# Optimization experiments

Hardware: AMD Instinct MI355X
Metric: run time of the kernel (lower is better)

Reference implementation:

```python
import jax, jax.numpy as jnp
import numpy as np

N = 100000
E = 1600000
D_IN = 128
HID = 128
N_CLASSES = 40
NEG_SLOPE = 0.2  # PyG GATConv default
BN_EPS = 1e-5


def setup_inputs() -> dict:
    key = jax.random.key(0)
    ks = jax.random.split(key, 16)
    s = 0.1
    return {
        "x": jax.random.normal(ks[0], (N, D_IN), dtype=jnp.float32),
        "edge_index": jax.random.randint(ks[1], (2, E), 0, N, dtype=jnp.int64),
        # GAT layer 1 (in=D_IN, out=HID, heads=1)
        "W1": jax.random.normal(ks[2], (D_IN, HID), dtype=jnp.float32) * s,
        "a_src1": jax.random.normal(ks[3], (HID,), dtype=jnp.float32) * s,
        "a_dst1": jax.random.normal(ks[4], (HID,), dtype=jnp.float32) * s,
        "b1": jnp.zeros((HID,), dtype=jnp.float32),
        # GAT layer 2 (in=HID, out=HID, heads=1)
        "W2": jax.random.normal(ks[5], (HID, HID), dtype=jnp.float32) * s,
        "a_src2": jax.random.normal(ks[6], (HID,), dtype=jnp.float32) * s,
        "a_dst2": jax.random.normal(ks[7], (HID,), dtype=jnp.float32) * s,
        "b2": jnp.zeros((HID,), dtype=jnp.float32),
        # shared BatchNorm1d(HID) applied after every conv
        "gamma": jnp.ones((HID,), dtype=jnp.float32),
        "beta": jnp.zeros((HID,), dtype=jnp.float32),
        # output Linear(HID, N_CLASSES)
        "Wout": jax.random.normal(ks[8], (HID, N_CLASSES), dtype=jnp.float32) * s,
        "bout": jnp.zeros((N_CLASSES,), dtype=jnp.float32),
    }


def reference(x, edge_index, W1, a_src1, a_dst1, b1, W2, a_src2, a_dst2, b2,
              gamma, beta, Wout, bout):
    n = x.shape[0]
    loops = jnp.arange(n, dtype=edge_index.dtype)  # add_self_loops (GATConv default)
    src = jnp.concatenate([edge_index[0], loops])
    dst = jnp.concatenate([edge_index[1], loops])

    def gat_layer(h_in, W, a_s, a_d, b):
        h = h_in @ W                                   # [N, HID]
        e_src = h @ a_s                                # [N] per-node src score
        e_dst = h @ a_d                                # [N] per-node dst score
        e = jax.nn.leaky_relu(e_src[src] + e_dst[dst], NEG_SLOPE)  # [E+N]
        # segment softmax over incoming edges of each dst node
        m = jax.ops.segment_max(e, dst, num_segments=n)
        p = jnp.exp(e - m[dst])
        denom = jax.ops.segment_sum(p, dst, num_segments=n)
        alpha = p / denom[dst]
        out = jax.ops.segment_sum(alpha[:, None] * h[src], dst, num_segments=n)
        return out + b

    def bn_elu(z):
        mu = z.mean(axis=0)
        var = ((z - mu) ** 2).mean(axis=0)  # biased var (BN training mode)
        zh = (z - mu) / jnp.sqrt(var + BN_EPS) * gamma + beta
        return jax.nn.elu(zh)

    h = bn_elu(gat_layer(x, W1, a_src1, a_dst1, b1))
    h = bn_elu(gat_layer(h, W2, a_src2, a_dst2, b2))
    return h @ Wout + bout
```

## Files before the change

kernel.cpp:

```cpp
#include <hip/hip_runtime.h>

#define NNODES 100000
#define NEDGES 1600000
#define ET (NEDGES + NNODES)
#define NBUCK 196
#define NEG 0.2f
#define BNEPS 1e-5f
#define EPB 16384
#define NBLK_E ((ET + EPB - 1) / EPB)

typedef __attribute__((ext_vector_type(8))) short short8;
typedef __attribute__((ext_vector_type(4))) float floatx4;
typedef __attribute__((ext_vector_type(2))) float floatx2;

__device__ __forceinline__ unsigned short f2b(float x) {
    unsigned int u = __float_as_uint(x);
    u += 0x7fff + ((u >> 16) & 1);
    return (unsigned short)(u >> 16);
}
__device__ __forceinline__ float b2f(unsigned short u) {
    return __uint_as_float(((unsigned int)u) << 16);
}
__device__ __forceinline__ float blo2f(unsigned int v) {
    return __uint_as_float(v << 16);
}
__device__ __forceinline__ float bhi2f(unsigned int v) {
    return __uint_as_float(v & 0xffff0000u);
}
__device__ __forceinline__ floatx2 u2f2(unsigned int v) {
    floatx2 r;
    r.x = __uint_as_float(v << 16);
    r.y = __uint_as_float(v & 0xffff0000u);
    return r;
}

__device__ __forceinline__ int edge_src(const int* ei, int e, int w64) {
    if (e >= NEDGES) return e - NEDGES;
    return w64 ? ei[2 * e] : ei[e];
}
__device__ __forceinline__ int edge_dst(const int* ei, int e, int w64) {
    if (e >= NEDGES) return e - NEDGES;
    return w64 ? ei[2 * (NEDGES + e)] : ei[NEDGES + e];
}

__global__ void k_prep(const float* __restrict__ W1, const float* __restrict__ W2,
                       unsigned short* __restrict__ WT1, unsigned short* __restrict__ WT2,
                       const int* ei, int* flag) {
    int t = blockIdx.x * 256 + threadIdx.x;
    if (t == 0) {
        int is64 = 1;
        for (int j = 1; j < 16; j += 2)
            if (ei[j] != 0) is64 = 0;
        *flag = is64;
    }
    int k = t >> 7, n = t & 127;
    WT1[n * 128 + k] = f2b(W1[t]);
    WT2[n * 128 + k] = f2b(W2[t]);
}

__global__ __launch_bounds__(256) void k_bhist(const int* __restrict__ ei,
                                               const int* flag, int* bcnt) {
    __shared__ int lc[256];
    int t = threadIdx.x;
    lc[t] = 0;
    __syncthreads();
    int w64 = *flag;
    int base = blockIdx.x * EPB;
    for (int j = 0; j < EPB / 256; j++) {
        int e = base + j * 256 + t;
        if (e < ET) atomicAdd(&lc[edge_dst(ei, e, w64) >> 9], 1);
    }
    __syncthreads();
    if (t < NBUCK && lc[t]) atomicAdd(&bcnt[t], lc[t]);
}

__global__ void k_bscan(const int* __restrict__ bcnt, int* bbase, int* bcur) {
    __shared__ int sh[256];
    int t = threadIdx.x;
    int v = (t < NBUCK) ? bcnt[t] : 0;
    sh[t] = v;
    __syncthreads();
    for (int off = 1; off < 256; off <<= 1) {
        int add = (t >= off) ? sh[t - off] : 0;
        __syncthreads();
        sh[t] += add;
        __syncthreads();
    }
    int excl = sh[t] - v;
    if (t < NBUCK) { bbase[t] = excl; bcur[t] = excl; }
    if (t == NBUCK - 1) bbase[NBUCK] = sh[t];
}

__global__ __launch_bounds__(256) void k_bscatter(const int* __restrict__ ei,
                                                  const int* flag, int* bcur,
                                                  int* __restrict__ pairs) {
    __shared__ int lc[256];
    __shared__ int lbase[256];
    int t = threadIdx.x;
    lc[t] = 0;
    __syncthreads();
    int w64 = *flag;
    int base = blockIdx.x * EPB;
    for (int j = 0; j < EPB / 256; j++) {
        int e = base + j * 256 + t;
        if (e < ET) atomicAdd(&lc[edge_dst(ei, e, w64) >> 9], 1);
    }
    __syncthreads();
    if (t < NBUCK && lc[t]) lbase[t] = atomicAdd(&bcur[t], lc[t]);
    __syncthreads();
    for (int j = 0; j < EPB / 256; j++) {
        int e = base + j * 256 + t;
        if (e < ET) {
            int src = edge_src(ei, e, w64);
            int dst = edge_dst(ei, e, w64);
            int pos = atomicAdd(&lbase[dst >> 9], 1);
            pairs[pos] = (src << 9) | (dst & 511);
        }
    }
}

__global__ __launch_bounds__(256) void k_bsort(const int* __restrict__ pairs,
                                               const int* __restrict__ bbase,
                                               int* __restrict__ rowptr,
                                               int* __restrict__ srcs) {
    __shared__ int ncnt[512];
    __shared__ int nbase[512];
    __shared__ int stmp[256];
    int b = blockIdx.x, t = threadIdx.x;
    ncnt[t] = 0; ncnt[t + 256] = 0;
    __syncthreads();
    int s0 = bbase[b], s1 = bbase[b + 1];
    for (int i = s0 + t; i < s1; i += 256)
        atomicAdd(&ncnt[pairs[i] & 511], 1);
    __syncthreads();
    int c0 = ncnt[2 * t], c1 = ncnt[2 * t + 1];
    int s = c0 + c1;
    stmp[t] = s;
    __syncthreads();
    for (int off = 1; off < 256; off <<= 1) {
        int add = (t >= off) ? stmp[t - off] : 0;
        __syncthreads();
        stmp[t] += add;
        __syncthreads();
    }
    int excl = stmp[t] - s;
    nbase[2 * t] = excl;
    nbase[2 * t + 1] = excl + c0;
    __syncthreads();
    for (int l = t; l < 512; l += 256) {
        int node = b * 512 + l;
        if (node <= NNODES) rowptr[node] = s0 + nbase[l];
        ncnt[l] = nbase[l];
    }
    __syncthreads();
    for (int i = s0 + t; i < s1; i += 256) {
        int pr = pairs[i];
        int off = atomicAdd(&ncnt[pr & 511], 1);
        srcs[s0 + off] = ((unsigned int)pr) >> 9;
    }
}

template<bool BN>
__global__ __launch_bounds__(256) void k_gemm(const void* __restrict__ Ain,
        const unsigned short* __restrict__ WTg,
        const float* __restrict__ sums, const float* __restrict__ sqs,
        const float* __restrict__ gamma, const float* __restrict__ beta,
        const float* __restrict__ a_s, const float* __restrict__ a_d,
        float* __restrict__ es, float* __restrict__ ed,
        unsigned short* __restrict__ hB, int n) {
    __shared__ unsigned short lA[64][136];
    __shared__ unsigned short lW[128][136];
    __shared__ float las[128], lad[128];
    __shared__ float lsc[128], lsh[128];
    int t = threadIdx.x;
    int row0 = blockIdx.x * 64;
    if (t < 128) { las[t] = a_s[t]; lad[t] = a_d[t]; }
    if (BN && t < 128) {
        float mu = sums[t] * (1.f / NNODES);
        float var = fmaxf(sqs[t] * (1.f / NNODES) - mu * mu, 0.f);
        float s = gamma[t] * rsqrtf(var + BNEPS);
        lsc[t] = s;
        lsh[t] = beta[t] - mu * s;
    }

    const uint4* wt4 = (const uint4*)WTg;
#pragma unroll
    for (int j = 0; j < 8; j++) {
        int idx = t + j * 256;
        *(uint4*)&lW[idx >> 4][(idx & 15) * 8] = wt4[idx];
    }
    if (BN) __syncthreads();

    if (BN) {
        const uint4* Ab = (const uint4*)Ain;
#pragma unroll
        for (int j = 0; j < 4; j++) {
            int idx = t + j * 256;
            int r = idx >> 4, seg = idx & 15;
            uint4 v = make_uint4(0, 0, 0, 0);
            if (row0 + r < n) v = Ab[(size_t)(row0 + r) * 16 + seg];
            float f[8];
            f[0] = blo2f(v.x); f[1] = bhi2f(v.x);
            f[2] = blo2f(v.y); f[3] = bhi2f(v.y);
            f[4] = blo2f(v.z); f[5] = bhi2f(v.z);
            f[6] = blo2f(v.w); f[7] = bhi2f(v.w);
            ushort4 u0, u1;
            unsigned short us[8];
#pragma unroll
            for (int k = 0; k < 8; k++) {
                int c = seg * 8 + k;
                float z = fmaf(f[k], lsc[c], lsh[c]);
                z = z > 0.f ? z : __expf(z) - 1.f;
                us[k] = f2b(z);
            }
            u0.x = us[0]; u0.y = us[1]; u0.z = us[2]; u0.w = us[3];
            u1.x = us[4]; u1.y = us[5]; u1.z = us[6]; u1.w = us[7];
            *(ushort4*)&lA[r][seg * 8] = u0;
            *(ushort4*)&lA[r][seg * 8 + 4] = u1;
        }
    } else {
        const float* Af = (const float*)Ain;
#pragma unroll
        for (int j = 0; j < 8; j++) {
            int idx = t + j * 256;
            int r = idx >> 5, c4 = idx & 31;
            float4 v = make_float4(0.f, 0.f, 0.f, 0.f);
            if (row0 + r < n) v = ((const float4*)Af)[(size_t)(row0 + r) * 32 + c4];
            ushort4 u;
            u.x = f2b(v.x); u.y = f2b(v.y); u.z = f2b(v.z); u.w = f2b(v.w);
            *(ushort4*)&lA[r][c4 * 4] = u;
        }
    }
    __syncthreads();

    int w = t >> 6, lane = t & 63;
    int m = lane & 15, q = lane >> 4;
    int arow = w * 16 + m;
    floatx4 acc[8];
#pragma unroll
    for (int ct = 0; ct < 8; ct++) acc[ct] = (floatx4)0.0f;

#pragma unroll
    for (int kt = 0; kt < 4; kt++) {
        int kb = kt * 32 + q * 8;
        short8 af = *(const short8*)&lA[arow][kb];
#pragma unroll
        for (int ct = 0; ct < 8; ct++) {
            short8 bf = *(const short8*)&lW[ct * 16 + m][kb];
            acc[ct] = __builtin_amdgcn_mfma_f32_16x16x32_bf16(af, bf, acc[ct], 0, 0, 0);
        }
    }

    __syncthreads();
#pragma unroll
    for (int ct = 0; ct < 8; ct++)
#pragma unroll
        for (int r = 0; r < 4; r++)
            lA[w * 16 + q * 4 + r][ct * 16 + m] = f2b(acc[ct][r]);
#pragma unroll
    for (int j = 0; j < 4; j++) {
        int idx = lane + j * 64;
        int r = idx >> 4, seg = idx & 15;
        int grow = row0 + w * 16 + r;
        if (grow < n) {
            uint4 v = *(const uint4*)&lA[w * 16 + r][seg * 8];
            ((uint4*)hB)[(size_t)grow * 16 + seg] = v;
        }
    }
    __syncthreads();
    int r = t >> 2, q4 = t & 3;
    float s1 = 0.f, s2 = 0.f;
#pragma unroll
    for (int k = 0; k < 32; k++) {
        int c = q4 * 32 + k;
        float v = b2f(lA[r][c]);
        s1 += v * las[c];
        s2 += v * lad[c];
    }
    s1 += __shfl_xor(s1, 1, 64); s1 += __shfl_xor(s1, 2, 64);
    s2 += __shfl_xor(s2, 1, 64); s2 += __shfl_xor(s2, 2, 64);
    if (q4 == 0 && row0 + r < n) { es[row0 + r] = s1; ed[row0 + r] = s2; }
}

__global__ __launch_bounds__(256) void k_attn(const unsigned short* __restrict__ hB,
                                              const int* __restrict__ srcs,
                                              const int* __restrict__ rowptr,
                                              const float* __restrict__ es,
                                              const float* __restrict__ ed,
                                              const float* __restrict__ bias,
                                              unsigned short* __restrict__ haggB, int n) {
    int w = (blockIdx.x * 256 + threadIdx.x) >> 5;
    if (w >= n) return;
    int lane32 = threadIdx.x & 31;
    int g = lane32 >> 4, l16 = lane32 & 15;
    int base = threadIdx.x & 32;
    int start = rowptr[w], end = rowptr[w + 1];
    float edv = ed[w];
    const uint4* hp4 = (const uint4*)hB;
    floatx2 a0 = {0.f, 0.f}, a1 = {0.f, 0.f}, a2 = {0.f, 0.f}, a3 = {0.f, 0.f};
    float den = 0.f;

    for (int chunk = start; chunk < end; chunk += 32) {
        int i = chunk + lane32;
        int sv = 0; float pv = 0.f;
        if (i < end) {
            sv = srcs[i];
            float e = es[sv] + edv;
            e = e > 0.f ? e : NEG * e;
            pv = __expf(e);
            den += pv;
        }
        int cnt = min(32, end - chunk);
        for (int j = 0; j < cnt; j += 4) {
            int   s0 = __shfl(sv, base + j + g, 64);
            float p0 = __shfl(pv, base + j + g, 64);
            int   s1 = __shfl(sv, base + j + 2 + g, 64);
            float p1 = __shfl(pv, base + j + 2 + g, 64);
            if (p0 != 0.f) {
                uint4 h0 = hp4[(size_t)s0 * 16 + l16];
                floatx2 P = {p0, p0};
                a0 += P * u2f2(h0.x); a1 += P * u2f2(h0.y);
                a2 += P * u2f2(h0.z); a3 += P * u2f2(h0.w);
            }
            if (p1 != 0.f) {
                uint4 h1 = hp4[(size_t)s1 * 16 + l16];
                floatx2 P = {p1, p1};
                a0 += P * u2f2(h1.x); a1 += P * u2f2(h1.y);
                a2 += P * u2f2(h1.z); a3 += P * u2f2(h1.w);
            }
        }
    }
    den += __shfl_xor(den, 1, 64);  den += __shfl_xor(den, 2, 64);
    den += __shfl_xor(den, 4, 64);  den += __shfl_xor(den, 8, 64);
    den += __shfl_xor(den, 16, 64);
    a0.x += __shfl_xor(a0.x, 16, 64); a0.y += __shfl_xor(a0.y, 16, 64);
    a1.x += __shfl_xor(a1.x, 16, 64); a1.y += __shfl_xor(a1.y, 16, 64);
    a2.x += __shfl_xor(a2.x, 16, 64); a2.y += __shfl_xor(a2.y, 16, 64);
    a3.x += __shfl_xor(a3.x, 16, 64); a3.y += __shfl_xor(a3.y, 16, 64);
    if (g == 0) {
        float inv = 1.f / den;
        const float2* b2 = (const float2*)bias;
        float2 c0 = b2[l16 * 4 + 0], c1 = b2[l16 * 4 + 1];
        float2 c2 = b2[l16 * 4 + 2], c3 = b2[l16 * 4 + 3];
        uint4 o;
        o.x = (unsigned int)f2b(fmaf(a0.x, inv, c0.x)) |
              ((unsigned int)f2b(fmaf(a0.y, inv, c0.y)) << 16);
        o.y = (unsigned int)f2b(fmaf(a1.x, inv, c1.x)) |
              ((unsigned int)f2b(fmaf(a1.y, inv, c1.y)) << 16);
        o.z = (unsigned int)f2b(fmaf(a2.x, inv, c2.x)) |
              ((unsigned int)f2b(fmaf(a2.y, inv, c2.y)) << 16);
        o.w = (unsigned int)f2b(fmaf(a3.x, inv, c3.x)) |
              ((unsigned int)f2b(fmaf(a3.y, inv, c3.y)) << 16);
        ((uint4*)haggB)[(size_t)w * 16 + l16] = o;
    }
}

__global__ __launch_bounds__(256) void k_bnstats(const unsigned short* __restrict__ hin,
                                                 float* sums, float* sqs, int n) {
    __shared__ float red[4][256];
    int t = threadIdx.x;
    int c2 = t & 63, quarter = t >> 6;
    int r0 = blockIdx.x * 512;
    int rend = min(r0 + 512, n);
    const unsigned int* hp = (const unsigned int*)hin;
    float s0 = 0.f, q0 = 0.f, s1 = 0.f, q1 = 0.f;
    for (int r = r0 + quarter; r < rend; r += 4) {
        unsigned int v = hp[(size_t)r * 64 + c2];
        float a = blo2f(v), b = bhi2f(v);
        s0 += a; q0 += a * a;
        s1 += b; q1 += b * b;
    }
    *(float4*)&red[quarter][c2 * 4] = make_float4(s0, q0, s1, q1);
    __syncthreads();
    float v = red[0][t] + red[1][t] + red[2][t] + red[3][t];
    int c2i = t >> 2, k = t & 3;
    int ch = c2i * 2 + (k >> 1);
    if (k & 1) atomicAdd(&sqs[ch], v);
    else       atomicAdd(&sums[ch], v);
}

__global__ __launch_bounds__(256) void k_outgemm(const unsigned short* __restrict__ h,
                                                 const float* __restrict__ sums,
                                                 const float* __restrict__ sqs,
                                                 const float* __restrict__ gamma,
                                                 const float* __restrict__ beta,
                                                 const float* __restrict__ Wout,
                                                 const float* __restrict__ bout,
                                                 float* __restrict__ out, int n) {
    __shared__ float lwT[40][128];
    __shared__ float lh[64][132];
    __shared__ float lb[40];
    __shared__ float lsc[128], lsh[128];
    int t = threadIdx.x;
    if (t < 128) {
        float mu = sums[t] * (1.f / NNODES);
        float var = fmaxf(sqs[t] * (1.f / NNODES) - mu * mu, 0.f);
        float s = gamma[t] * rsqrtf(var + BNEPS);
        lsc[t] = s;
        lsh[t] = beta[t] - mu * s;
    }
    for (int idx = t; idx < 128 * 40; idx += 256) {
        int r = idx / 40, c = idx % 40;
        lwT[c][r] = Wout[idx];
    }
    if (t < 40) lb[t] = bout[t];
    __syncthreads();
    int n0 = blockIdx.x * 64;
    const uint4* hb4 = (const uint4*)h;
#pragma unroll
    for (int j = 0; j < 4; j++) {
        int idx = t + j * 256;
        int r = idx >> 4, seg = idx & 15;
        uint4 v = make_uint4(0, 0, 0, 0);
        if (n0 + r < n) v = hb4[(size_t)(n0 + r) * 16 + seg];
        float f[8];
        f[0] = blo2f(v.x); f[1] = bhi2f(v.x);
        f[2] = blo2f(v.y); f[3] = bhi2f(v.y);
        f[4] = blo2f(v.z); f[5] = bhi2f(v.z);
        f[6] = blo2f(v.w); f[7] = bhi2f(v.w);
#pragma unroll
        for (int k = 0; k < 8; k++) {
            int c = seg * 8 + k;
            float z = fmaf(f[k], lsc[c], lsh[c]);
            z = z > 0.f ? z : __expf(z) - 1.f;
            lh[r][c] = z;
        }
    }
    __syncthreads();
    int nl = t & 63, g = t >> 6;
    int row = n0 + nl;
    if (row >= n) return;
    float acc[10] = {};
    for (int k = 0; k < 128; k += 4) {
        float4 hv = *(const float4*)&lh[nl][k];
#pragma unroll
        for (int j = 0; j < 10; j++) {
            float4 wv = *(const float4*)&lwT[g * 10 + j][k];
            acc[j] += hv.x * wv.x + hv.y * wv.y + hv.z * wv.z + hv.w * wv.w;
        }
    }
#pragma unroll
    for (int j = 0; j < 10; j++)
        out[(size_t)row * 40 + g * 10 + j] = acc[j] + lb[g * 10 + j];
}

extern "C" void kernel_launch(void* const* d_in, const int* in_sizes, int n_in,
                              void* d_out, int out_size, void* d_ws, size_t ws_size,
                              hipStream_t stream) {
    const float* x      = (const float*)d_in[0];
    const int*   ei     = (const int*)d_in[1];
    const float* W1     = (const float*)d_in[2];
    const float* a_src1 = (const float*)d_in[3];
    const float* a_dst1 = (const float*)d_in[4];
    const float* b1     = (const float*)d_in[5];
    const float* W2     = (const float*)d_in[6];
    const float* a_src2 = (const float*)d_in[7];
    const float* a_dst2 = (const float*)d_in[8];
    const float* b2     = (const float*)d_in[9];
    const float* gamma  = (const float*)d_in[10];
    const float* beta   = (const float*)d_in[11];
    const float* Wout   = (const float*)d_in[12];
    const float* bout   = (const float*)d_in[13];
    float* out = (float*)d_out;

    char* p = (char*)d_ws;
    auto alloc = [&](size_t bytes) -> void* {
        void* r = (void*)p;
        p += (bytes + 255) & ~(size_t)255;
        return r;
    };
    unsigned short* hB    = (unsigned short*)alloc((size_t)NNODES * 128 * 2);
    unsigned short* haggB = (unsigned short*)alloc((size_t)NNODES * 128 * 2);
    float* es     = (float*)alloc((size_t)NNODES * 4);
    float* ed     = (float*)alloc((size_t)NNODES * 4);
    int*   pairs  = (int*)alloc((size_t)ET * 4);
    int*   srcs   = (int*)alloc((size_t)ET * 4);
    int*   rowptr = (int*)alloc((size_t)(NNODES + 1) * 4);
    int*   bcnt   = (int*)alloc(256 * 4);
    int*   bbase  = (int*)alloc(256 * 4);
    int*   bcur   = (int*)alloc(256 * 4);
    float* bnstat = (float*)alloc(4 * 128 * 4);
    unsigned short* WT1 = (unsigned short*)alloc(128 * 128 * 2);
    unsigned short* WT2 = (unsigned short*)alloc(128 * 128 * 2);
    int*   flag   = (int*)alloc(4);

    float* sum1 = bnstat, *sq1 = bnstat + 128, *sum2 = bnstat + 256, *sq2 = bnstat + 384;

    hipMemsetAsync(bcnt, 0, 256 * 4, stream);
    hipMemsetAsync(bnstat, 0, 4 * 128 * 4, stream);

    k_prep<<<64, 256, 0, stream>>>(W1, W2, WT1, WT2, ei, flag);
    k_bhist<<<NBLK_E, 256, 0, stream>>>(ei, flag, bcnt);
    k_bscan<<<1, 256, 0, stream>>>(bcnt, bbase, bcur);
    k_bscatter<<<NBLK_E, 256, 0, stream>>>(ei, flag, bcur, pairs);
    k_bsort<<<NBUCK, 256, 0, stream>>>(pairs, bbase, rowptr, srcs);

    const int GB = (NNODES + 63) / 64;
    const int AB = NNODES / 8;
    const int SB = (NNODES + 511) / 512;

    k_gemm<false><<<GB, 256, 0, stream>>>(x, WT1, nullptr, nullptr, nullptr, nullptr,
                                          a_src1, a_dst1, es, ed, hB, NNODES);
    k_attn<<<AB, 256, 0, stream>>>(hB, srcs, rowptr, es, ed, b1, haggB, NNODES);
    k_bnstats<<<SB, 256, 0, stream>>>(haggB, sum1, sq1, NNODES);

    k_gemm<true><<<GB, 256, 0, stream>>>(haggB, WT2, sum1, sq1, gamma, beta,
                                         a_src2, a_dst2, es, ed, hB, NNODES);
    k_attn<<<AB, 256, 0, stream>>>(hB, srcs, rowptr, es, ed, b2, haggB, NNODES);
    k_bnstats<<<SB, 256, 0, stream>>>(haggB, sum2, sq2, NNODES);

    k_outgemm<<<GB, 256, 0, stream>>>(haggB, sum2, sq2, gamma, beta, Wout, bout, out, NNODES);

    (void)in_sizes; (void)n_in; (void)out_size; (void)ws_size;
}
```

Before: 491.7 us.

## Fold memsets and scan into kernels, vectorize edge reads, use 16 lanes per node

Zeroing of the bucket counters and BN stats moves into the weight-prep kernel. The single-block bucket scan is merged into the histogram kernel through a last-block-done counter, which removes two memsets and one launch. Edge index reads in the histogram and scatter passes are vectorized to two edges per thread. The attention aggregation now gives each node 16 lanes instead of 32, with one source row per iteration, and drops the zero-weight skip and the cross-half reduction. The aim is to cut launch overhead and improve occupancy and latency hiding for the typical degree of about 17. In exchange it relies on atomic and threadfence ordering for the fused scan, and each node now has fewer loads in flight.

Result: no change. 485.3 us (-1.3%).

```diff
diff --git a/kernel.cpp b/kernel.cpp
--- a/kernel.cpp
+++ b/kernel.cpp
@@ -45,13 +45,21 @@
 
 __global__ void k_prep(const float* __restrict__ W1, const float* __restrict__ W2,
                        unsigned short* __restrict__ WT1, unsigned short* __restrict__ WT2,
-                       const int* ei, int* flag) {
+                       const int* ei, int* flag, int* bcnt, int* done, float* bnstat) {
     int t = blockIdx.x * 256 + threadIdx.x;
-    if (t == 0) {
-        int is64 = 1;
-        for (int j = 1; j < 16; j += 2)
-            if (ei[j] != 0) is64 = 0;
-        *flag = is64;
+    if (blockIdx.x == 0) {
+        bcnt[threadIdx.x] = 0;
+        if (threadIdx.x == 0) *done = 0;
+        if (threadIdx.x == 1) {
+            int is64 = 1;
+            for (int j = 1; j < 16; j += 2)
+                if (ei[j] != 0) is64 = 0;
+            *flag = is64;
+        }
+    } else if (blockIdx.x == 1) {
+        bnstat[threadIdx.x] = 0.f;
+    } else if (blockIdx.x == 2) {
+        bnstat[256 + threadIdx.x] = 0.f;
     }
     int k = t >> 7, n = t & 127;
     WT1[n * 128 + k] = f2b(W1[t]);
@@ -59,36 +67,55 @@
 }
 
 __global__ __launch_bounds__(256) void k_bhist(const int* __restrict__ ei,
-                                               const int* flag, int* bcnt) {
+                                               const int* flag, int* bcnt,
+                                               int* done, int* bbase, int* bcur) {
     __shared__ int lc[256];
+    __shared__ int lastf;
     int t = threadIdx.x;
     lc[t] = 0;
     __syncthreads();
     int w64 = *flag;
     int base = blockIdx.x * EPB;
-    for (int j = 0; j < EPB / 256; j++) {
-        int e = base + j * 256 + t;
-        if (e < ET) atomicAdd(&lc[edge_dst(ei, e, w64) >> 9], 1);
+    for (int j = 0; j < EPB / 512; j++) {
+        int e = base + j * 512 + t * 2;
+        if (e + 1 < NEDGES) {
+            int d0, d1;
+            if (w64) {
+                int4 dv = *(const int4*)&ei[2 * (NEDGES + e)];
+                d0 = dv.x; d1 = dv.z;
+            } else {
+                int2 dv = *(const int2*)&ei[NEDGES + e];
+                d0 = dv.x; d1 = dv.y;
+            }
+            atomicAdd(&lc[d0 >> 9], 1);
+            atomicAdd(&lc[d1 >> 9], 1);
+        } else {
+            for (int k = 0; k < 2; k++) {
+                int ee = e + k;
+                if (ee < ET) atomicAdd(&lc[edge_dst(ei, ee, w64) >> 9], 1);
+            }
+        }
     }
     __syncthreads();
     if (t < NBUCK && lc[t]) atomicAdd(&bcnt[t], lc[t]);
-}
-
-__global__ void k_bscan(const int* __restrict__ bcnt, int* bbase, int* bcur) {
-    __shared__ int sh[256];
-    int t = threadIdx.x;
-    int v = (t < NBUCK) ? bcnt[t] : 0;
-    sh[t] = v;
+    __threadfence();
+    __syncthreads();
+    if (t == 0) lastf = (atomicAdd(done, 1) == gridDim.x - 1) ? 1 : 0;
+    __syncthreads();
+    if (!lastf) return;
+    int v = (t < NBUCK) ? atomicAdd(&bcnt[t], 0) : 0;
+    __syncthreads();
+    lc[t] = v;
     __syncthreads();
     for (int off = 1; off < 256; off <<= 1) {
-        int add = (t >= off) ? sh[t - off] : 0;
+        int add = (t >= off) ? lc[t - off] : 0;
         __syncthreads();
-        sh[t] += add;
+        lc[t] += add;
         __syncthreads();
     }
-    int excl = sh[t] - v;
+    int excl = lc[t] - v;
     if (t < NBUCK) { bbase[t] = excl; bcur[t] = excl; }
-    if (t == NBUCK - 1) bbase[NBUCK] = sh[t];
+    if (t == NBUCK - 1) bbase[NBUCK] = excl + v;
 }
 
 __global__ __launch_bounds__(256) void k_bscatter(const int* __restrict__ ei,
@@ -101,20 +128,56 @@
     __syncthreads();
     int w64 = *flag;
     int base = blockIdx.x * EPB;
-    for (int j = 0; j < EPB / 256; j++) {
-        int e = base + j * 256 + t;
-        if (e < ET) atomicAdd(&lc[edge_dst(ei, e, w64) >> 9], 1);
+    for (int j = 0; j < EPB / 512; j++) {
+        int e = base + j * 512 + t * 2;
+        if (e + 1 < NEDGES) {
+            int d0, d1;
+            if (w64) {
+                int4 dv = *(const int4*)&ei[2 * (NEDGES + e)];
+                d0 = dv.x; d1 = dv.z;
+            } else {
+                int2 dv = *(const int2*)&ei[NEDGES + e];
+                d0 = dv.x; d1 = dv.y;
+            }
+            atomicAdd(&lc[d0 >> 9], 1);
+            atomicAdd(&lc[d1 >> 9], 1);
+        } else {
+            for (int k = 0; k < 2; k++) {
+                int ee = e + k;
+                if (ee < ET) atomicAdd(&lc[edge_dst(ei, ee, w64) >> 9], 1);
+            }
+        }
     }
     __syncthreads();
     if (t < NBUCK && lc[t]) lbase[t] = atomicAdd(&bcur[t], lc[t]);
     __syncthreads();
-    for (int j = 0; j < EPB / 256; j++) {
-        int e = base + j * 256 + t;
-        if (e < ET) {
-            int src = edge_src(ei, e, w64);
-            int dst = edge_dst(ei, e, w64);
-            int pos = atomicAdd(&lbase[dst >> 9], 1);
-            pairs[pos] = (src << 9) | (dst & 511);
+    for (int j = 0; j < EPB / 512; j++) {
+        int e = base + j * 512 + t * 2;
+        if (e + 1 < NEDGES) {
+            int s0, s1, d0, d1;
+            if (w64) {
+                int4 sv = *(const int4*)&ei[2 * e];
+                int4 dv = *(const int4*)&ei[2 * (NEDGES + e)];
+                s0 = sv.x; s1 = sv.z; d0 = dv.x; d1 = dv.z;
+            } else {
+                int2 sv = *(const int2*)&ei[e];
+                int2 dv = *(const int2*)&ei[NEDGES + e];
+                s0 = sv.x; s1 = sv.y; d0 = dv.x; d1 = dv.y;
+            }
+            int p0 = atomicAdd(&lbase[d0 >> 9], 1);
+            pairs[p0] = (s0 << 9) | (d0 & 511);
+            int p1 = atomicAdd(&lbase[d1 >> 9], 1);
+            pairs[p1] = (s1 << 9) | (d1 & 511);
+        } else {
+            for (int k = 0; k < 2; k++) {
+                int ee = e + k;
+                if (ee < ET) {
+                    int src = edge_src(ei, ee, w64);
+                    int dst = edge_dst(ei, ee, w64);
+                    int pos = atomicAdd(&lbase[dst >> 9], 1);
+                    pairs[pos] = (src << 9) | (dst & 511);
+                }
+            }
         }
     }
 }
@@ -289,19 +352,18 @@
                                               const float* __restrict__ ed,
                                               const float* __restrict__ bias,
                                               unsigned short* __restrict__ haggB, int n) {
-    int w = (blockIdx.x * 256 + threadIdx.x) >> 5;
+    int w = (blockIdx.x * 256 + threadIdx.x) >> 4;
     if (w >= n) return;
-    int lane32 = threadIdx.x & 31;
-    int g = lane32 >> 4, l16 = lane32 & 15;
-    int base = threadIdx.x & 32;
+    int l = threadIdx.x & 15;
+    int qb = threadIdx.x & 48;
     int start = rowptr[w], end = rowptr[w + 1];
     float edv = ed[w];
     const uint4* hp4 = (const uint4*)hB;
     floatx2 a0 = {0.f, 0.f}, a1 = {0.f, 0.f}, a2 = {0.f, 0.f}, a3 = {0.f, 0.f};
     float den = 0.f;
 
-    for (int chunk = start; chunk < end; chunk += 32) {
-        int i = chunk + lane32;
+    for (int chunk = start; chunk < end; chunk += 16) {
+        int i = chunk + l;
         int sv = 0; float pv = 0.f;
         if (i < end) {
             sv = srcs[i];
@@ -310,49 +372,32 @@
             pv = __expf(e);
             den += pv;
         }
-        int cnt = min(32, end - chunk);
-        for (int j = 0; j < cnt; j += 4) {
-            int   s0 = __shfl(sv, base + j + g, 64);
-            float p0 = __shfl(pv, base + j + g, 64);
-            int   s1 = __shfl(sv, base + j + 2 + g, 64);
-            float p1 = __shfl(pv, base + j + 2 + g, 64);
-            if (p0 != 0.f) {
-                uint4 h0 = hp4[(size_t)s0 * 16 + l16];
-                floatx2 P = {p0, p0};
-                a0 += P * u2f2(h0.x); a1 += P * u2f2(h0.y);
-                a2 += P * u2f2(h0.z); a3 += P * u2f2(h0.w);
-            }
-            if (p1 != 0.f) {
-                uint4 h1 = hp4[(size_t)s1 * 16 + l16];
-                floatx2 P = {p1, p1};
-                a0 += P * u2f2(h1.x); a1 += P * u2f2(h1.y);
-                a2 += P * u2f2(h1.z); a3 += P * u2f2(h1.w);
-            }
-        }
-    }
-    den += __shfl_xor(den, 1, 64);  den += __shfl_xor(den, 2, 64);
-    den += __shfl_xor(den, 4, 64);  den += __shfl_xor(den, 8, 64);
-    den += __shfl_xor(den, 16, 64);
-    a0.x += __shfl_xor(a0.x, 16, 64); a0.y += __shfl_xor(a0.y, 16, 64);
-    a1.x += __shfl_xor(a1.x, 16, 64); a1.y += __shfl_xor(a1.y, 16, 64);
-    a2.x += __shfl_xor(a2.x, 16, 64); a2.y += __shfl_xor(a2.y, 16, 64);
-    a3.x += __shfl_xor(a3.x, 16, 64); a3.y += __shfl_xor(a3.y, 16, 64);
-    if (g == 0) {
-        float inv = 1.f / den;
-        const float2* b2 = (const float2*)bias;
-        float2 c0 = b2[l16 * 4 + 0], c1 = b2[l16 * 4 + 1];
-        float2 c2 = b2[l16 * 4 + 2], c3 = b2[l16 * 4 + 3];
-        uint4 o;
-        o.x = (unsigned int)f2b(fmaf(a0.x, inv, c0.x)) |
-              ((unsigned int)f2b(fmaf(a0.y, inv, c0.y)) << 16);
-        o.y = (unsigned int)f2b(fmaf(a1.x, inv, c1.x)) |
-              ((unsigned int)f2b(fmaf(a1.y, inv, c1.y)) << 16);
-        o.z = (unsigned int)f2b(fmaf(a2.x, inv, c2.x)) |
-              ((unsigned int)f2b(fmaf(a2.y, inv, c2.y)) << 16);
-        o.w = (unsigned int)f2b(fmaf(a3.x, inv, c3.x)) |
-              ((unsigned int)f2b(fmaf(a3.y, inv, c3.y)) << 16);
-        ((uint4*)haggB)[(size_t)w * 16 + l16] = o;
-    }
+        int cnt = min(16, end - chunk);
+        for (int j = 0; j < cnt; j++) {
+            int   s0 = __shfl(sv, qb + j, 64);
+            float p0 = __shfl(pv, qb + j, 64);
+            uint4 h0 = hp4[(size_t)s0 * 16 + l];
+            floatx2 P = {p0, p0};
+            a0 += P * u2f2(h0.x); a1 += P * u2f2(h0.y);
+            a2 += P * u2f2(h0.z); a3 += P * u2f2(h0.w);
+        }
+    }
+    den += __shfl_xor(den, 1, 64); den += __shfl_xor(den, 2, 64);
+    den += __shfl_xor(den, 4, 64); den += __shfl_xor(den, 8, 64);
+    float inv = 1.f / den;
+    const float2* b2p = (const float2*)bias;
+    float2 c0 = b2p[l * 4 + 0], c1 = b2p[l * 4 + 1];
+    float2 c2 = b2p[l * 4 + 2], c3 = b2p[l * 4 + 3];
+    uint4 o;
+    o.x = (unsigned int)f2b(fmaf(a0.x, inv, c0.x)) |
+          ((unsigned int)f2b(fmaf(a0.y, inv, c0.y)) << 16);
+    o.y = (unsigned int)f2b(fmaf(a1.x, inv, c1.x)) |
+          ((unsigned int)f2b(fmaf(a1.y, inv, c1.y)) << 16);
+    o.z = (unsigned int)f2b(fmaf(a2.x, inv, c2.x)) |
+          ((unsigned int)f2b(fmaf(a2.y, inv, c2.y)) << 16);
+    o.w = (unsigned int)f2b(fmaf(a3.x, inv, c3.x)) |
+          ((unsigned int)f2b(fmaf(a3.y, inv, c3.y)) << 16);
+    ((uint4*)haggB)[(size_t)w * 16 + l] = o;
 }
 
 __global__ __launch_bounds__(256) void k_bnstats(const unsigned short* __restrict__ hin,
@@ -483,20 +528,17 @@
     unsigned short* WT1 = (unsigned short*)alloc(128 * 128 * 2);
     unsigned short* WT2 = (unsigned short*)alloc(128 * 128 * 2);
     int*   flag   = (int*)alloc(4);
+    int*   done   = (int*)alloc(4);
 
     float* sum1 = bnstat, *sq1 = bnstat + 128, *sum2 = bnstat + 256, *sq2 = bnstat + 384;
 
-    hipMemsetAsync(bcnt, 0, 256 * 4, stream);
-    hipMemsetAsync(bnstat, 0, 4 * 128 * 4, stream);
-
-    k_prep<<<64, 256, 0, stream>>>(W1, W2, WT1, WT2, ei, flag);
-    k_bhist<<<NBLK_E, 256, 0, stream>>>(ei, flag, bcnt);
-    k_bscan<<<1, 256, 0, stream>>>(bcnt, bbase, bcur);
+    k_prep<<<64, 256, 0, stream>>>(W1, W2, WT1, WT2, ei, flag, bcnt, done, bnstat);
+    k_bhist<<<NBLK_E, 256, 0, stream>>>(ei, flag, bcnt, done, bbase, bcur);
     k_bscatter<<<NBLK_E, 256, 0, stream>>>(ei, flag, bcur, pairs);
     k_bsort<<<NBUCK, 256, 0, stream>>>(pairs, bbase, rowptr, srcs);
 
     const int GB = (NNODES + 63) / 64;
-    const int AB = NNODES / 8;
+    const int AB = NNODES / 16;
     const int SB = (NNODES + 511) / 512;
 
     k_gemm<false><<<GB, 256, 0, stream>>>(x, WT1, nullptr, nullptr, nullptr, nullptr,
```
